# Kernel optimization log

Hardware: AMD Instinct MI355X
Metric: run time of the kernel (lower is better)

## Reference

```python
import jax, jax.numpy as jnp
import numpy as np

SEQ_LEN = 720
PRED_LEN = 720
RANK = 16
CTX_DIM = 128
HID = 64
BATCH = 256


def setup_inputs() -> dict:
    key = jax.random.key(0)
    ks = jax.random.split(key, 8)
    x = jax.random.normal(ks[0], (BATCH, SEQ_LEN, 1), dtype=jnp.float32)
    ctx = jax.random.normal(ks[1], (BATCH, CTX_DIM), dtype=jnp.float32)
    # Base weight, xavier-uniform init
    limit = np.sqrt(6.0 / (PRED_LEN + SEQ_LEN)).astype(np.float32)
    W = jax.random.uniform(ks[2], (PRED_LEN, SEQ_LEN), dtype=jnp.float32,
                           minval=-limit, maxval=limit)
    # hyper MLP: Linear(ctx_dim, 64) -> ReLU -> Linear(64, rank*(seq+pred))
    out_dim = RANK * (SEQ_LEN + PRED_LEN)
    b1_lim = 1.0 / np.sqrt(CTX_DIM)
    W1 = jax.random.uniform(ks[3], (HID, CTX_DIM), dtype=jnp.float32, minval=-b1_lim, maxval=b1_lim)
    b1 = jax.random.uniform(ks[4], (HID,), dtype=jnp.float32, minval=-b1_lim, maxval=b1_lim)
    b2_lim = 1.0 / np.sqrt(HID)
    W2 = jax.random.uniform(ks[5], (out_dim, HID), dtype=jnp.float32, minval=-b2_lim, maxval=b2_lim)
    b2 = jax.random.uniform(ks[6], (out_dim,), dtype=jnp.float32, minval=-b2_lim, maxval=b2_lim)
    return {"x": x, "ctx": ctx, "W": W, "W1": W1, "b1": b1, "W2": W2, "b2": b2}


def reference(x, ctx, W, W1, b1, W2, b2):
    B = x.shape[0]
    # hyper MLP
    h = jax.nn.relu(ctx @ W1.T + b1) @ W2.T + b2  # (B, rank*(seq+pred))
    A_delta = h[:, : RANK * PRED_LEN].reshape(B, PRED_LEN, RANK)
    B_delta = h[:, RANK * PRED_LEN:].reshape(B, RANK, SEQ_LEN)
    # per-sample effective weight (materialized, as in the original)
    W_eff = W[None] + jnp.einsum('bpr,brs->bps', A_delta, B_delta)  # (B, pred, seq)
    y = jnp.einsum('bps,bs->bp', W_eff, x[..., 0])  # (B, pred)
    return (y[..., None], W_eff)
```

## Files before the change

kernel.cpp:

```cpp
#include <hip/hip_runtime.h>

#define SEQ  720
#define PRED 720
#define RANK 16
#define CTXD 128
#define HID  64
#define BATCH 256
#define ODIM  (RANK * (SEQ + PRED))
#define ASIZE (RANK * PRED)

typedef float v4f __attribute__((ext_vector_type(4)));

__global__ __launch_bounds__(64) void k_hidden(const float* __restrict__ ctx,
                                               const float* __restrict__ W1,
                                               const float* __restrict__ b1,
                                               float* __restrict__ hid)
{
    __shared__ alignas(16) float cl[CTXD];
    int b = blockIdx.x, k = threadIdx.x;
    cl[k]      = ctx[b * CTXD + k];
    cl[k + 64] = ctx[b * CTXD + k + 64];
    __syncthreads();
    float acc = b1[k];
    const float* wr = W1 + k * CTXD;
#pragma unroll
    for (int c = 0; c < CTXD; c += 4) {
        float4 w  = *(const float4*)(wr + c);
        float4 xv = *(const float4*)(cl + c);
        acc = fmaf(w.x, xv.x, acc);
        acc = fmaf(w.y, xv.y, acc);
        acc = fmaf(w.z, xv.z, acc);
        acc = fmaf(w.w, xv.w, acc);
    }
    hid[b * HID + k] = fmaxf(acc, 0.0f);
}

__global__ __launch_bounds__(256) void k_hyper(const float* __restrict__ hid,
                                               const float* __restrict__ W2,
                                               const float* __restrict__ b2,
                                               float* __restrict__ h)
{
    int ot = blockIdx.x, bt = blockIdx.y;
    __shared__ alignas(16) float Hl[64 * 68];
    __shared__ alignas(16) float Wl[64 * 68];
    int tid = threadIdx.x;

    const float* hg = hid + (size_t)bt * 64 * HID;
    const float* wg = W2  + (size_t)ot * 64 * HID;
#pragma unroll
    for (int n = 0; n < 4; n++) {
        int g = tid * 4 + n * 1024;
        float4 hv = *(const float4*)(hg + g);
        float4 wv = *(const float4*)(wg + g);
        int row = g >> 6, colk = g & 63;
        *(float4*)&Hl[row * 68 + colk] = hv;
        *(float4*)&Wl[row * 68 + colk] = wv;
    }
    __syncthreads();

    int tx = tid & 15, ty = tid >> 4;
    float c[4][4];
#pragma unroll
    for (int j = 0; j < 4; j++) {
        float bv = b2[ot * 64 + j * 16 + tx];
        c[0][j] = bv; c[1][j] = bv; c[2][j] = bv; c[3][j] = bv;
    }
#pragma unroll
    for (int kc = 0; kc < HID; kc += 4) {
        float4 hv[4], wv[4];
#pragma unroll
        for (int i = 0; i < 4; i++) hv[i] = *(const float4*)&Hl[(ty * 4 + i) * 68 + kc];
#pragma unroll
        for (int j = 0; j < 4; j++) wv[j] = *(const float4*)&Wl[(j * 16 + tx) * 68 + kc];
#pragma unroll
        for (int i = 0; i < 4; i++)
#pragma unroll
            for (int j = 0; j < 4; j++) {
                c[i][j] = fmaf(hv[i].x, wv[j].x, c[i][j]);
                c[i][j] = fmaf(hv[i].y, wv[j].y, c[i][j]);
                c[i][j] = fmaf(hv[i].z, wv[j].z, c[i][j]);
                c[i][j] = fmaf(hv[i].w, wv[j].w, c[i][j]);
            }
    }
#pragma unroll
    for (int i = 0; i < 4; i++) {
        int b = bt * 64 + ty * 4 + i;
        float* hb = h + (size_t)b * ODIM + ot * 64;
#pragma unroll
        for (int j = 0; j < 4; j++)
            hb[j * 16 + tx] = c[i][j];
    }
}

#define FMA4(ci, av, bv)                 \
    ci.x = fmaf(av, bv.x, ci.x);         \
    ci.y = fmaf(av, bv.y, ci.y);         \
    ci.z = fmaf(av, bv.z, ci.z);         \
    ci.w = fmaf(av, bv.w, ci.w);

__global__ __launch_bounds__(256) void k_weff(const float* __restrict__ h,
                                              const float* __restrict__ W,
                                              const float* __restrict__ x,
                                              float* __restrict__ y,
                                              float* __restrict__ weff)
{
    int st = blockIdx.x, pt = blockIdx.y, b = blockIdx.z;
    __shared__ alignas(16) float Al[64 * 20];
    __shared__ alignas(16) float Bl[16 * 64];
    __shared__ float Yr[64 * 17];
    int tid = threadIdx.x;
    const float* hb = h + (size_t)b * ODIM;

    {
        int g = tid * 4;
        int p = pt * 64 + (g >> 4);
        float4 v = make_float4(0.f, 0.f, 0.f, 0.f);
        if (p < PRED) v = *(const float4*)(hb + pt * 1024 + g);
        *(float4*)&Al[(g >> 4) * 20 + (g & 15)] = v;
    }
    {
        int r = tid >> 4, sl = (tid & 15) * 4, s = st * 64 + sl;
        float4 v = make_float4(0.f, 0.f, 0.f, 0.f);
        if (s < SEQ) v = *(const float4*)(hb + ASIZE + r * SEQ + s);
        *(float4*)&Bl[r * 64 + sl] = v;
    }
    __syncthreads();

    int tx = tid & 15, ty = tid >> 4;
    int sl = tx * 4, s = st * 64 + sl;
    bool sv = (s < SEQ);
    int p0 = pt * 64 + ty * 4;

    float4 c[4];
#pragma unroll
    for (int i = 0; i < 4; i++) c[i] = make_float4(0.f, 0.f, 0.f, 0.f);

#pragma unroll
    for (int rc = 0; rc < RANK; rc += 4) {
        float4 bb[4];
#pragma unroll
        for (int j = 0; j < 4; j++) bb[j] = *(const float4*)&Bl[(rc + j) * 64 + sl];
#pragma unroll
        for (int i = 0; i < 4; i++) {
            float4 a = *(const float4*)&Al[(ty * 4 + i) * 20 + rc];
            FMA4(c[i], a.x, bb[0]);
            FMA4(c[i], a.y, bb[1]);
            FMA4(c[i], a.z, bb[2]);
            FMA4(c[i], a.w, bb[3]);
        }
    }

    float4 xv = make_float4(0.f, 0.f, 0.f, 0.f);
    if (sv) xv = *(const float4*)(x + b * SEQ + s);

#pragma unroll
    for (int i = 0; i < 4; i++) {
        int p = p0 + i;
        float yp = 0.0f;
        if (sv && p < PRED) {
            float4 wv = *(const float4*)(W + (size_t)p * SEQ + s);
            v4f e;
            e.x = wv.x + c[i].x;
            e.y = wv.y + c[i].y;
            e.z = wv.z + c[i].z;
            e.w = wv.w + c[i].w;
            __builtin_nontemporal_store(e,
                (v4f*)(weff + (size_t)b * ((size_t)PRED * SEQ) + (size_t)p * SEQ + s));
            yp = e.x * xv.x + e.y * xv.y + e.z * xv.z + e.w * xv.w;
        }
        Yr[(ty * 4 + i) * 17 + tx] = yp;
    }
    __syncthreads();
    if (tid < 64) {
        float sum = 0.0f;
#pragma unroll
        for (int t = 0; t < 16; t++) sum += Yr[tid * 17 + t];
        int p = pt * 64 + tid;
        if (p < PRED) atomicAdd(y + (size_t)b * PRED + p, sum);
    }
}

extern "C" void kernel_launch(void* const* d_in, const int* in_sizes, int n_in,
                              void* d_out, int out_size, void* d_ws, size_t ws_size,
                              hipStream_t stream)
{
    const float* x   = (const float*)d_in[0];
    const float* ctx = (const float*)d_in[1];
    const float* W   = (const float*)d_in[2];
    const float* W1  = (const float*)d_in[3];
    const float* b1  = (const float*)d_in[4];
    const float* W2  = (const float*)d_in[5];
    const float* b2  = (const float*)d_in[6];

    float* out  = (float*)d_out;
    float* yout = out;
    float* weff = out + (size_t)BATCH * PRED;

    float* hid = (float*)d_ws;
    float* h   = hid + (size_t)BATCH * HID;

    (void)hipMemsetAsync(yout, 0, (size_t)BATCH * PRED * sizeof(float), stream);

    k_hidden<<<dim3(BATCH), dim3(64), 0, stream>>>(ctx, W1, b1, hid);
    k_hyper<<<dim3(ODIM / 64, BATCH / 64), dim3(256), 0, stream>>>(hid, W2, b2, h);
    k_weff<<<dim3(12, 12, BATCH), dim3(256), 0, stream>>>(h, W, x, yout, weff);
}
```

Before: 640.0 us.

## Retile W_eff kernel to wave-per-row strips with shuffle-reduced y

Changes the k_weff tile from 64x64 to 48 pred rows by 256 seq columns. Each wave now owns 12 full rows, and each lane covers 4 contiguous columns, so stores are full 1 KB rows per wave instruction. The per-row y partial is reduced with wave shuffles and one atomic per wave, replacing the shared-memory reduction and the second barrier. This makes stores more contiguous and cuts block count and sync overhead. In exchange it uses more registers per thread (12 float4 accumulators), and the last seq tile leaves 48 of its 256 columns idle.

Measured after the change: 845.4 us. 32.1% more time.

```diff
diff --git a/kernel.cpp b/kernel.cpp
--- a/kernel.cpp
+++ b/kernel.cpp
@@ -9,7 +9,17 @@
 #define ODIM  (RANK * (SEQ + PRED))
 #define ASIZE (RANK * PRED)
 
+#define PT 48
+#define ST 256
+#define RPW (PT / 4)
+
 typedef float v4f __attribute__((ext_vector_type(4)));
+
+#define FMA4(ci, av, bv)                 \
+    ci.x = fmaf(av, bv.x, ci.x);         \
+    ci.y = fmaf(av, bv.y, ci.y);         \
+    ci.z = fmaf(av, bv.z, ci.z);         \
+    ci.w = fmaf(av, bv.w, ci.w);
 
 __global__ __launch_bounds__(64) void k_hidden(const float* __restrict__ ctx,
                                                const float* __restrict__ W1,
@@ -92,91 +102,81 @@
     }
 }
 
-#define FMA4(ci, av, bv)                 \
-    ci.x = fmaf(av, bv.x, ci.x);         \
-    ci.y = fmaf(av, bv.y, ci.y);         \
-    ci.z = fmaf(av, bv.z, ci.z);         \
-    ci.w = fmaf(av, bv.w, ci.w);
-
 __global__ __launch_bounds__(256) void k_weff(const float* __restrict__ h,
                                               const float* __restrict__ W,
                                               const float* __restrict__ x,
                                               float* __restrict__ y,
                                               float* __restrict__ weff)
 {
-    int st = blockIdx.x, pt = blockIdx.y, b = blockIdx.z;
-    __shared__ alignas(16) float Al[64 * 20];
-    __shared__ alignas(16) float Bl[16 * 64];
-    __shared__ float Yr[64 * 17];
-    int tid = threadIdx.x;
+    const int st = blockIdx.x, pt = blockIdx.y, b = blockIdx.z;
+    const int s0 = st * ST, p0 = pt * PT;
+    __shared__ alignas(16) float Al[PT * RANK];
+    __shared__ alignas(16) float Bl[RANK][ST];
+    const int tid = threadIdx.x;
     const float* hb = h + (size_t)b * ODIM;
 
+    if (tid < (PT * RANK / 4))
+        *(float4*)&Al[tid * 4] = *(const float4*)(hb + p0 * RANK + tid * 4);
+
     {
-        int g = tid * 4;
-        int p = pt * 64 + (g >> 4);
-        float4 v = make_float4(0.f, 0.f, 0.f, 0.f);
-        if (p < PRED) v = *(const float4*)(hb + pt * 1024 + g);
-        *(float4*)&Al[(g >> 4) * 20 + (g & 15)] = v;
-    }
-    {
-        int r = tid >> 4, sl = (tid & 15) * 4, s = st * 64 + sl;
-        float4 v = make_float4(0.f, 0.f, 0.f, 0.f);
-        if (s < SEQ) v = *(const float4*)(hb + ASIZE + r * SEQ + s);
-        *(float4*)&Bl[r * 64 + sl] = v;
+        const int r = tid >> 4, c4 = tid & 15;
+        const float* brow = hb + ASIZE + r * SEQ;
+#pragma unroll
+        for (int q = 0; q < 4; q++) {
+            int col = q * 64 + c4 * 4;
+            float4 v = make_float4(0.f, 0.f, 0.f, 0.f);
+            if (s0 + col < SEQ) v = *(const float4*)(brow + s0 + col);
+            *(float4*)&Bl[r][col] = v;
+        }
     }
     __syncthreads();
 
-    int tx = tid & 15, ty = tid >> 4;
-    int sl = tx * 4, s = st * 64 + sl;
-    bool sv = (s < SEQ);
-    int p0 = pt * 64 + ty * 4;
-
-    float4 c[4];
-#pragma unroll
-    for (int i = 0; i < 4; i++) c[i] = make_float4(0.f, 0.f, 0.f, 0.f);
+    const int wave = tid >> 6, lane = tid & 63;
+    const int s = s0 + lane * 4;
+    const bool sv = (s < SEQ);
+    const int pbase = p0 + wave * RPW;
+
+    float4 c[RPW];
+#pragma unroll
+    for (int k = 0; k < RPW; k++) c[k] = make_float4(0.f, 0.f, 0.f, 0.f);
 
 #pragma unroll
     for (int rc = 0; rc < RANK; rc += 4) {
         float4 bb[4];
 #pragma unroll
-        for (int j = 0; j < 4; j++) bb[j] = *(const float4*)&Bl[(rc + j) * 64 + sl];
-#pragma unroll
-        for (int i = 0; i < 4; i++) {
-            float4 a = *(const float4*)&Al[(ty * 4 + i) * 20 + rc];
-            FMA4(c[i], a.x, bb[0]);
-            FMA4(c[i], a.y, bb[1]);
-            FMA4(c[i], a.z, bb[2]);
-            FMA4(c[i], a.w, bb[3]);
+        for (int j = 0; j < 4; j++) bb[j] = *(const float4*)&Bl[rc + j][lane * 4];
+#pragma unroll
+        for (int k = 0; k < RPW; k++) {
+            float4 a = *(const float4*)&Al[(wave * RPW + k) * RANK + rc];
+            FMA4(c[k], a.x, bb[0]);
+            FMA4(c[k], a.y, bb[1]);
+            FMA4(c[k], a.z, bb[2]);
+            FMA4(c[k], a.w, bb[3]);
         }
     }
 
     float4 xv = make_float4(0.f, 0.f, 0.f, 0.f);
-    if (sv) xv = *(const float4*)(x + b * SEQ + s);
-
-#pragma unroll
-    for (int i = 0; i < 4; i++) {
-        int p = p0 + i;
-        float yp = 0.0f;
-        if (sv && p < PRED) {
+    if (sv) xv = *(const float4*)(x + (size_t)b * SEQ + s);
+
+    float* wb = weff + (size_t)b * ((size_t)PRED * SEQ);
+#pragma unroll
+    for (int k = 0; k < RPW; k++) {
+        const int p = pbase + k;
+        float part = 0.0f;
+        if (sv) {
             float4 wv = *(const float4*)(W + (size_t)p * SEQ + s);
             v4f e;
-            e.x = wv.x + c[i].x;
-            e.y = wv.y + c[i].y;
-            e.z = wv.z + c[i].z;
-            e.w = wv.w + c[i].w;
-            __builtin_nontemporal_store(e,
-                (v4f*)(weff + (size_t)b * ((size_t)PRED * SEQ) + (size_t)p * SEQ + s));
-            yp = e.x * xv.x + e.y * xv.y + e.z * xv.z + e.w * xv.w;
+            e.x = wv.x + c[k].x;
+            e.y = wv.y + c[k].y;
+            e.z = wv.z + c[k].z;
+            e.w = wv.w + c[k].w;
+            __builtin_nontemporal_store(e, (v4f*)(wb + (size_t)p * SEQ + s));
+            part = e.x * xv.x + e.y * xv.y + e.z * xv.z + e.w * xv.w;
         }
-        Yr[(ty * 4 + i) * 17 + tx] = yp;
-    }
-    __syncthreads();
-    if (tid < 64) {
-        float sum = 0.0f;
-#pragma unroll
-        for (int t = 0; t < 16; t++) sum += Yr[tid * 17 + t];
-        int p = pt * 64 + tid;
-        if (p < PRED) atomicAdd(y + (size_t)b * PRED + p, sum);
+#pragma unroll
+        for (int m = 32; m > 0; m >>= 1)
+            part += __shfl_xor(part, m, 64);
+        if (lane == 0) atomicAdd(y + (size_t)b * PRED + p, part);
     }
 }
 
@@ -203,5 +203,5 @@
 
     k_hidden<<<dim3(BATCH), dim3(64), 0, stream>>>(ctx, W1, b1, hid);
     k_hyper<<<dim3(ODIM / 64, BATCH / 64), dim3(256), 0, stream>>>(hid, W2, b2, h);
-    k_weff<<<dim3(12, 12, BATCH), dim3(256), 0, stream>>>(h, W, x, yout, weff);
-}
+    k_weff<<<dim3(SEQ / ST + 1, PRED / PT, BATCH), dim3(256), 0, stream>>>(h, W, x, yout, weff);
+}
```
